# Performance work log

Measured on AMD Instinct MI355X. Metric: run time of the kernel, lower is better.

The kernel has to match this reference:

```python
import jax, jax.numpy as jnp
import numpy as np

THRESHOLD = 0.5
DILATION_ITERS = 5  # scipy binary_dilation(iterations=5)


def _dilate_cross(mask, iters=DILATION_ITERS):
    # mask: [T, H, W] bool. scipy's default 3D structure on a [H,W,1] frame
    # degenerates to a 2D 4-connected (cross) structuring element.
    # One iteration = OR of center and the 4 axis-aligned neighbors.
    for _ in range(iters):
        p = jnp.pad(mask, ((0, 0), (1, 1), (1, 1)))
        mask = (p[:, 1:-1, 1:-1]
                | p[:, :-2, 1:-1] | p[:, 2:, 1:-1]
                | p[:, 1:-1, :-2] | p[:, 1:-1, 2:])
    return mask


def setup_inputs() -> dict:
    key = jax.random.key(0)
    k1, k2 = jax.random.split(key)
    X = jax.random.normal(k1, (3, 128, 256, 256), dtype=jnp.float32)          # [C,T,H,W]
    background = jax.random.normal(k2, (256, 256, 3), dtype=jnp.float32)      # [H,W,C]
    return {"X": X, "background": background}


def reference(X, background):
    Xp = jnp.transpose(X, (1, 2, 3, 0))                                       # [T,H,W,C]
    mask = jnp.sum(jnp.abs(Xp - background), axis=-1) > THRESHOLD             # [T,H,W]
    mask = _dilate_cross(mask)
    out = Xp * mask[..., None].astype(Xp.dtype)
    return jnp.transpose(out, (3, 0, 1, 2))                                   # [C,T,H,W]
```

## Files before the change

kernel.cpp:

```cpp
#include <hip/hip_runtime.h>
#include <stdint.h>

#define TT 128
#define HH 256
#define WW 256
#define PLANE (TT*HH*WW)
#define FRAME (HH*WW)
#define ROWS 32
#define TPF  (HH/ROWS)
#define REPEAT 4
#define HALO 5
#define BROWS (ROWS + 2*HALO)
#define THRESH 0.5f

typedef float nfloat4 __attribute__((ext_vector_type(4)));

__device__ __forceinline__ uint64_t shfl64(uint64_t v, int src) {
    uint32_t lo = (uint32_t)v, hi = (uint32_t)(v >> 32);
    lo = __shfl(lo, src);
    hi = __shfl(hi, src);
    return ((uint64_t)hi << 32) | lo;
}

__device__ __forceinline__ uint64_t pack16(uint32_t nib) {
    int lane = threadIdx.x & 63;
    uint64_t v = (uint64_t)nib << (4 * (lane & 15));
    v |= __shfl_xor(v, 1);
    v |= __shfl_xor(v, 2);
    v |= __shfl_xor(v, 4);
    v |= __shfl_xor(v, 8);
    return v;
}

__device__ __forceinline__ uint32_t mask_nib(const float* __restrict__ X,
                                             const float* __restrict__ bg,
                                             int t, int gr, int col4) {
    if (gr < 0 || gr >= HH) return 0u;
    size_t pix = (size_t)t * FRAME + (size_t)gr * WW + 4 * col4;
    nfloat4 x0 = *(const nfloat4*)(X + pix);
    nfloat4 x1 = *(const nfloat4*)(X + (size_t)PLANE + pix);
    nfloat4 x2 = *(const nfloat4*)(X + 2 * (size_t)PLANE + pix);
    const nfloat4* bp = (const nfloat4*)(bg + ((size_t)gr * WW + 4 * col4) * 3);
    nfloat4 q0 = bp[0], q1 = bp[1], q2 = bp[2];
    uint32_t nib = 0;
    nib |= ((fabsf(x0[0] - q0[0]) + fabsf(x1[0] - q0[1]) + fabsf(x2[0] - q0[2])) > THRESH) ? 1u : 0u;
    nib |= ((fabsf(x0[1] - q0[3]) + fabsf(x1[1] - q1[0]) + fabsf(x2[1] - q1[1])) > THRESH) ? 2u : 0u;
    nib |= ((fabsf(x0[2] - q1[2]) + fabsf(x1[2] - q1[3]) + fabsf(x2[2] - q2[0])) > THRESH) ? 4u : 0u;
    nib |= ((fabsf(x0[3] - q2[1]) + fabsf(x1[3] - q2[2]) + fabsf(x2[3] - q2[3])) > THRESH) ? 8u : 0u;
    return nib;
}

__global__ __launch_bounds__(512) void fused_kernel(const float* __restrict__ X,
                                                    const float* __restrict__ bg,
                                                    float* __restrict__ out) {
    __shared__ uint64_t mbuf[2][BROWS][4];
    const int t    = blockIdx.x >> 1;
    const int j0   = (blockIdx.x & 1) * REPEAT;
    const int tid  = threadIdx.x;
    const int lane = tid & 63;
    const int wave = tid >> 6;
    const int col4 = lane;

#pragma unroll
    for (int rep = 0; rep < REPEAT; ++rep) {
        const int r0 = (j0 + rep) * ROWS;
        uint64_t (*B)[4] = mbuf[rep & 1];

        nfloat4 xv[4][3];
        uint32_t nib[4];
#pragma unroll
        for (int k = 0; k < 4; ++k) {
            const int gr = r0 + wave + 8 * k;
            size_t pix = (size_t)t * FRAME + (size_t)gr * WW + 4 * col4;
            xv[k][0] = *(const nfloat4*)(X + pix);
            xv[k][1] = *(const nfloat4*)(X + (size_t)PLANE + pix);
            xv[k][2] = *(const nfloat4*)(X + 2 * (size_t)PLANE + pix);
            const nfloat4* bp = (const nfloat4*)(bg + ((size_t)gr * WW + 4 * col4) * 3);
            nfloat4 q0 = bp[0], q1 = bp[1], q2 = bp[2];
            uint32_t nb = 0;
            nb |= ((fabsf(xv[k][0][0] - q0[0]) + fabsf(xv[k][1][0] - q0[1]) + fabsf(xv[k][2][0] - q0[2])) > THRESH) ? 1u : 0u;
            nb |= ((fabsf(xv[k][0][1] - q0[3]) + fabsf(xv[k][1][1] - q1[0]) + fabsf(xv[k][2][1] - q1[1])) > THRESH) ? 2u : 0u;
            nb |= ((fabsf(xv[k][0][2] - q1[2]) + fabsf(xv[k][1][2] - q1[3]) + fabsf(xv[k][2][2] - q2[0])) > THRESH) ? 4u : 0u;
            nb |= ((fabsf(xv[k][0][3] - q2[1]) + fabsf(xv[k][1][3] - q2[2]) + fabsf(xv[k][2][3] - q2[3])) > THRESH) ? 8u : 0u;
            nib[k] = nb;
        }
#pragma unroll
        for (int k = 0; k < 4; ++k) {
            uint64_t w = pack16(nib[k]);
            if ((lane & 15) == 0) B[HALO + wave + 8 * k][lane >> 4] = w;
        }
        {
            const int slot = wave;
            const int gr   = (slot < 5) ? (r0 - HALO + slot) : (r0 + ROWS + (slot - 5));
            const int brow = (slot < 5) ? slot : (HALO + ROWS + (slot - 5));
            uint64_t w = pack16(mask_nib(X, bg, t, gr, col4));
            if ((lane & 15) == 0) B[brow][lane >> 4] = w;
        }
        if (tid < 128) {
            const int slot = 8 + wave;
            const int gr   = r0 + ROWS + (slot - 5);
            const int brow = HALO + ROWS + (slot - 5);
            uint64_t w = pack16(mask_nib(X, bg, t, gr, col4));
            if ((lane & 15) == 0) B[brow][lane >> 4] = w;
        }
        __syncthreads();

        uint64_t r_[4];
#pragma unroll
        for (int i = 0; i < 4; ++i) r_[i] = (lane < BROWS) ? B[lane][i] : 0ULL;
#pragma unroll
        for (int it = 0; it < 5; ++it) {
            uint64_t nr[4];
#pragma unroll
            for (int i = 0; i < 4; ++i) {
                uint64_t c  = r_[i];
                uint64_t l  = (i > 0) ? r_[i - 1] : 0ULL;
                uint64_t rr = (i < 3) ? r_[i + 1] : 0ULL;
                uint64_t u  = shfl64(c, lane - 1);
                uint64_t d  = shfl64(c, lane + 1);
                u = (lane == 0) ? 0ULL : u;
                nr[i] = c | (c << 1) | (l >> 63) | (c >> 1) | (rr << 63) | u | d;
            }
#pragma unroll
            for (int i = 0; i < 4; ++i) r_[i] = nr[i];
        }

#pragma unroll
        for (int k = 0; k < 4; ++k) {
            const int row = wave + 8 * k;
            const int src = HALO + row;
            uint64_t t0 = shfl64(r_[0], src);
            uint64_t t1 = shfl64(r_[1], src);
            uint64_t t2 = shfl64(r_[2], src);
            uint64_t t3 = shfl64(r_[3], src);
            const int idx = lane >> 4;
            uint64_t lo = (idx & 1) ? t1 : t0;
            uint64_t hi = (idx & 1) ? t3 : t2;
            uint64_t w  = (idx & 2) ? hi : lo;
            uint32_t nb = (uint32_t)(w >> (4 * (lane & 15))) & 0xFu;
            float m0 = (float)(nb & 1u);
            float m1 = (float)((nb >> 1) & 1u);
            float m2 = (float)((nb >> 2) & 1u);
            float m3 = (float)((nb >> 3) & 1u);
            size_t pix = (size_t)t * FRAME + (size_t)(r0 + row) * WW + 4 * col4;
#pragma unroll
            for (int c = 0; c < 3; ++c) {
                nfloat4 v = xv[k][c];
                nfloat4 nv = { v[0] * m0, v[1] * m1, v[2] * m2, v[3] * m3 };
                __builtin_nontemporal_store(nv, (nfloat4*)(out + (size_t)c * PLANE + pix));
            }
        }
    }
}

extern "C" void kernel_launch(void* const* d_in, const int* in_sizes, int n_in,
                              void* d_out, int out_size, void* d_ws, size_t ws_size,
                              hipStream_t stream) {
    const float* X  = (const float*)d_in[0];
    const float* bg = (const float*)d_in[1];
    float* out = (float*)d_out;
    const int nblocks = TT * (TPF / REPEAT);
    fused_kernel<<<nblocks, 512, 0, stream>>>(X, bg, out);
}
```

Measured before the change: 44.16 us.

## Halve rows per block, issue halo loads early, dilate in one wave

Each block now covers 2 row-tiles instead of 4, which doubles the grid to 512 blocks so more CUs are busy. All X loads for the main rows and the halo rows are issued before any mask arithmetic, so their memory latency overlaps. The 5-step cross dilation runs only in wave 0 and writes its result back to shared memory, where every wave reads its mask bits. This drops the redundant dilation in the other 7 waves and the shuffle-based broadcast, at the cost of an extra __syncthreads and the other waves idling while wave 0 dilates.

```diff
diff --git a/kernel.cpp b/kernel.cpp
--- a/kernel.cpp
+++ b/kernel.cpp
@@ -8,7 +8,8 @@
 #define FRAME (HH*WW)
 #define ROWS 32
 #define TPF  (HH/ROWS)
-#define REPEAT 4
+#define REPEAT 2
+#define GROUPS (TPF/REPEAT)
 #define HALO 5
 #define BROWS (ROWS + 2*HALO)
 #define THRESH 0.5f
@@ -32,14 +33,9 @@
     return v;
 }
 
-__device__ __forceinline__ uint32_t mask_nib(const float* __restrict__ X,
+__device__ __forceinline__ uint32_t nib_from(nfloat4 x0, nfloat4 x1, nfloat4 x2,
                                              const float* __restrict__ bg,
-                                             int t, int gr, int col4) {
-    if (gr < 0 || gr >= HH) return 0u;
-    size_t pix = (size_t)t * FRAME + (size_t)gr * WW + 4 * col4;
-    nfloat4 x0 = *(const nfloat4*)(X + pix);
-    nfloat4 x1 = *(const nfloat4*)(X + (size_t)PLANE + pix);
-    nfloat4 x2 = *(const nfloat4*)(X + 2 * (size_t)PLANE + pix);
+                                             int gr, int col4) {
     const nfloat4* bp = (const nfloat4*)(bg + ((size_t)gr * WW + 4 * col4) * 3);
     nfloat4 q0 = bp[0], q1 = bp[1], q2 = bp[2];
     uint32_t nib = 0;
@@ -54,8 +50,8 @@
                                                     const float* __restrict__ bg,
                                                     float* __restrict__ out) {
     __shared__ uint64_t mbuf[2][BROWS][4];
-    const int t    = blockIdx.x >> 1;
-    const int j0   = (blockIdx.x & 1) * REPEAT;
+    const int t    = blockIdx.x >> 2;
+    const int j0   = (blockIdx.x & (GROUPS - 1)) * REPEAT;
     const int tid  = threadIdx.x;
     const int lane = tid & 63;
     const int wave = tid >> 6;
@@ -67,7 +63,6 @@
         uint64_t (*B)[4] = mbuf[rep & 1];
 
         nfloat4 xv[4][3];
-        uint32_t nib[4];
 #pragma unroll
         for (int k = 0; k < 4; ++k) {
             const int gr = r0 + wave + 8 * k;
@@ -75,69 +70,79 @@
             xv[k][0] = *(const nfloat4*)(X + pix);
             xv[k][1] = *(const nfloat4*)(X + (size_t)PLANE + pix);
             xv[k][2] = *(const nfloat4*)(X + 2 * (size_t)PLANE + pix);
-            const nfloat4* bp = (const nfloat4*)(bg + ((size_t)gr * WW + 4 * col4) * 3);
-            nfloat4 q0 = bp[0], q1 = bp[1], q2 = bp[2];
-            uint32_t nb = 0;
-            nb |= ((fabsf(xv[k][0][0] - q0[0]) + fabsf(xv[k][1][0] - q0[1]) + fabsf(xv[k][2][0] - q0[2])) > THRESH) ? 1u : 0u;
-            nb |= ((fabsf(xv[k][0][1] - q0[3]) + fabsf(xv[k][1][1] - q1[0]) + fabsf(xv[k][2][1] - q1[1])) > THRESH) ? 2u : 0u;
-            nb |= ((fabsf(xv[k][0][2] - q1[2]) + fabsf(xv[k][1][2] - q1[3]) + fabsf(xv[k][2][2] - q2[0])) > THRESH) ? 4u : 0u;
-            nb |= ((fabsf(xv[k][0][3] - q2[1]) + fabsf(xv[k][1][3] - q2[2]) + fabsf(xv[k][2][3] - q2[3])) > THRESH) ? 8u : 0u;
-            nib[k] = nb;
         }
-#pragma unroll
-        for (int k = 0; k < 4; ++k) {
-            uint64_t w = pack16(nib[k]);
-            if ((lane & 15) == 0) B[HALO + wave + 8 * k][lane >> 4] = w;
+        const int slotA = wave;
+        const int grA   = (slotA < 5) ? (r0 - HALO + slotA) : (r0 + ROWS + (slotA - 5));
+        const int browA = (slotA < 5) ? slotA : (HALO + ROWS + (slotA - 5));
+        const bool okA  = (grA >= 0) && (grA < HH);
+        nfloat4 ha0 = 0, ha1 = 0, ha2 = 0;
+        if (okA) {
+            size_t pix = (size_t)t * FRAME + (size_t)grA * WW + 4 * col4;
+            ha0 = *(const nfloat4*)(X + pix);
+            ha1 = *(const nfloat4*)(X + (size_t)PLANE + pix);
+            ha2 = *(const nfloat4*)(X + 2 * (size_t)PLANE + pix);
         }
-        {
-            const int slot = wave;
-            const int gr   = (slot < 5) ? (r0 - HALO + slot) : (r0 + ROWS + (slot - 5));
-            const int brow = (slot < 5) ? slot : (HALO + ROWS + (slot - 5));
-            uint64_t w = pack16(mask_nib(X, bg, t, gr, col4));
-            if ((lane & 15) == 0) B[brow][lane >> 4] = w;
-        }
-        if (tid < 128) {
-            const int slot = 8 + wave;
-            const int gr   = r0 + ROWS + (slot - 5);
-            const int brow = HALO + ROWS + (slot - 5);
-            uint64_t w = pack16(mask_nib(X, bg, t, gr, col4));
-            if ((lane & 15) == 0) B[brow][lane >> 4] = w;
-        }
-        __syncthreads();
-
-        uint64_t r_[4];
-#pragma unroll
-        for (int i = 0; i < 4; ++i) r_[i] = (lane < BROWS) ? B[lane][i] : 0ULL;
-#pragma unroll
-        for (int it = 0; it < 5; ++it) {
-            uint64_t nr[4];
-#pragma unroll
-            for (int i = 0; i < 4; ++i) {
-                uint64_t c  = r_[i];
-                uint64_t l  = (i > 0) ? r_[i - 1] : 0ULL;
-                uint64_t rr = (i < 3) ? r_[i + 1] : 0ULL;
-                uint64_t u  = shfl64(c, lane - 1);
-                uint64_t d  = shfl64(c, lane + 1);
-                u = (lane == 0) ? 0ULL : u;
-                nr[i] = c | (c << 1) | (l >> 63) | (c >> 1) | (rr << 63) | u | d;
-            }
-#pragma unroll
-            for (int i = 0; i < 4; ++i) r_[i] = nr[i];
+        const int grB   = r0 + ROWS + 3 + wave;
+        const int browB = HALO + ROWS + 3 + wave;
+        const bool okB  = (wave < 2) && (grB < HH);
+        nfloat4 hb0 = 0, hb1 = 0, hb2 = 0;
+        if (okB) {
+            size_t pix = (size_t)t * FRAME + (size_t)grB * WW + 4 * col4;
+            hb0 = *(const nfloat4*)(X + pix);
+            hb1 = *(const nfloat4*)(X + (size_t)PLANE + pix);
+            hb2 = *(const nfloat4*)(X + 2 * (size_t)PLANE + pix);
         }
 
 #pragma unroll
         for (int k = 0; k < 4; ++k) {
+            const int gr = r0 + wave + 8 * k;
+            uint64_t w = pack16(nib_from(xv[k][0], xv[k][1], xv[k][2], bg, gr, col4));
+            if ((lane & 15) == 0) B[HALO + wave + 8 * k][lane >> 4] = w;
+        }
+        {
+            uint32_t nb = okA ? nib_from(ha0, ha1, ha2, bg, grA, col4) : 0u;
+            uint64_t w = pack16(nb);
+            if ((lane & 15) == 0) B[browA][lane >> 4] = w;
+        }
+        if (wave < 2) {
+            uint32_t nb = okB ? nib_from(hb0, hb1, hb2, bg, grB, col4) : 0u;
+            uint64_t w = pack16(nb);
+            if ((lane & 15) == 0) B[browB][lane >> 4] = w;
+        }
+        __syncthreads();
+
+        if (wave == 0) {
+            uint64_t r_[4];
+#pragma unroll
+            for (int i = 0; i < 4; ++i) r_[i] = (lane < BROWS) ? B[lane][i] : 0ULL;
+#pragma unroll
+            for (int it = 0; it < 5; ++it) {
+                uint64_t nr[4];
+#pragma unroll
+                for (int i = 0; i < 4; ++i) {
+                    uint64_t c  = r_[i];
+                    uint64_t l  = (i > 0) ? r_[i - 1] : 0ULL;
+                    uint64_t rr = (i < 3) ? r_[i + 1] : 0ULL;
+                    uint64_t u  = shfl64(c, lane - 1);
+                    uint64_t d  = shfl64(c, lane + 1);
+                    u = (lane == 0) ? 0ULL : u;
+                    nr[i] = c | (c << 1) | (l >> 63) | (c >> 1) | (rr << 63) | u | d;
+                }
+#pragma unroll
+                for (int i = 0; i < 4; ++i) r_[i] = nr[i];
+            }
+            if (lane >= HALO && lane < HALO + ROWS) {
+#pragma unroll
+                for (int i = 0; i < 4; ++i) B[lane][i] = r_[i];
+            }
+        }
+        __syncthreads();
+
+#pragma unroll
+        for (int k = 0; k < 4; ++k) {
             const int row = wave + 8 * k;
-            const int src = HALO + row;
-            uint64_t t0 = shfl64(r_[0], src);
-            uint64_t t1 = shfl64(r_[1], src);
-            uint64_t t2 = shfl64(r_[2], src);
-            uint64_t t3 = shfl64(r_[3], src);
-            const int idx = lane >> 4;
-            uint64_t lo = (idx & 1) ? t1 : t0;
-            uint64_t hi = (idx & 1) ? t3 : t2;
-            uint64_t w  = (idx & 2) ? hi : lo;
-            uint32_t nb = (uint32_t)(w >> (4 * (lane & 15))) & 0xFu;
+            uint64_t w = B[HALO + row][col4 >> 4];
+            uint32_t nb = (uint32_t)(w >> (4 * (col4 & 15))) & 0xFu;
             float m0 = (float)(nb & 1u);
             float m1 = (float)((nb >> 1) & 1u);
             float m2 = (float)((nb >> 2) & 1u);
@@ -159,6 +164,6 @@
     const float* X  = (const float*)d_in[0];
     const float* bg = (const float*)d_in[1];
     float* out = (float*)d_out;
-    const int nblocks = TT * (TPF / REPEAT);
+    const int nblocks = TT * GROUPS;
     fused_kernel<<<nblocks, 512, 0, stream>>>(X, bg, out);
 }
```

Result: faster. 40.75 us (-7.7%).
